# Optimization experiments

Measured on AMD Instinct MI355X. Metric: run time of the kernel, lower is better.

The kernel has to match this reference:

```python
import jax, jax.numpy as jnp
import numpy as np

NHEADS = 16
KVHEADS = 4
HEAD_DIM = 128  # emb_kq_per_head == emb_v_per_head
ROPE_THETA = 10000.0


def _rotary(x, cos, sin):
    # x: [B, S, H, D]; half-split rotation
    x1, x2 = jnp.split(x, 2, axis=-1)
    rot = jnp.concatenate([-x2, x1], axis=-1)
    return x * cos + rot * sin


def setup_inputs() -> dict:
    key = jax.random.key(0)
    k1, k2, k3 = jax.random.split(key, 3)
    B, S, E = 2, 2048, 2048
    qkv_out = NHEADS * HEAD_DIM + 2 * KVHEADS * HEAD_DIM  # 3072
    return {
        "x": jax.random.normal(k1, (B, S, E), dtype=jnp.float32),
        "w_qkv": jax.random.normal(k2, (E, qkv_out), dtype=jnp.float32) * 0.02,
        "w_dense": jax.random.normal(k3, (NHEADS * HEAD_DIM, E), dtype=jnp.float32) * 0.02,
    }


def reference(x, w_qkv, w_dense):
    B, S, E = x.shape
    D = HEAD_DIM
    # fused QKV projection (use_bias=False), then split per FusedQKV.splits
    qkv = x @ w_qkv  # [B, S, 3072]
    q, k, v = jnp.split(qkv, [NHEADS * D, NHEADS * D + KVHEADS * D], axis=-1)
    q = q.reshape(B, S, NHEADS, D)
    k = k.reshape(B, S, KVHEADS, D)
    v = v.reshape(B, S, KVHEADS, D)

    # rotary position encoding, positions = arange(S)
    pos = jnp.arange(S, dtype=jnp.float32)
    inv_freq = 1.0 / (ROPE_THETA ** (jnp.arange(0, D, 2, dtype=jnp.float32) / D))
    ang = pos[:, None] * inv_freq[None, :]                 # [S, D/2]
    ang = jnp.concatenate([ang, ang], axis=-1)             # [S, D]
    cos = jnp.cos(ang)[None, :, None, :]                   # [1, S, 1, D]
    sin = jnp.sin(ang)[None, :, None, :]
    q = _rotary(q, cos, sin)
    k = _rotary(k, cos, sin)

    # GQA: expand kv heads to query heads
    rep = NHEADS // KVHEADS
    k = jnp.repeat(k, rep, axis=2)  # [B, S, NHEADS, D]
    v = jnp.repeat(v, rep, axis=2)

    scale = 1.0 / jnp.sqrt(jnp.asarray(D, dtype=x.dtype))
    scores = jnp.einsum("bqhd,bkhd->bhqk", q, k) * scale   # [B, H, S, S]
    causal = jnp.tril(jnp.ones((S, S), dtype=bool))
    scores = jnp.where(causal[None, None], scores, jnp.finfo(scores.dtype).min)
    probs = jax.nn.softmax(scores, axis=-1)
    attn = jnp.einsum("bhqk,bkhd->bqhd", probs, v)         # [B, S, H, D]
    attn = attn.reshape(B, S, NHEADS * D)
    return attn @ w_dense                                  # [B, S, E]
```

## Files before the change

### kernel.cpp

```cpp
#include <hip/hip_runtime.h>
#include <type_traits>


typedef __attribute__((ext_vector_type(8))) short short8;
typedef __attribute__((ext_vector_type(4))) float floatx4;
typedef __attribute__((ext_vector_type(4))) unsigned short ushort4v;
typedef __attribute__((ext_vector_type(4))) unsigned int uint4v;

constexpr int NH    = 16;
constexpr int NKV   = 4;
constexpr int HD    = 128;
constexpr int SEQ   = 2048;
constexpr int EMB   = 2048;
constexpr int NBATCH = 2;
constexpr int MROWS = NBATCH * SEQ;
constexpr int NQKV  = (NH + 2 * NKV) * HD;

__device__ __forceinline__ unsigned short f2b(float f) {
  union { float f; unsigned u; } v; v.f = f;
  unsigned u = v.u + 0x7FFFu + ((v.u >> 16) & 1u);
  return (unsigned short)(u >> 16);
}
__device__ __forceinline__ float b2f(unsigned short h) {
  union { unsigned u; float f; } v; v.u = (unsigned)h << 16;
  return v.f;
}

__device__ __forceinline__ void gload_lds16(const unsigned short* g,
                                            unsigned short* lds) {
  __builtin_amdgcn_global_load_lds(
      (const __attribute__((address_space(1))) unsigned int*)g,
      (__attribute__((address_space(3))) unsigned int*)lds, 16, 0, 0);
}

constexpr int PREP_CVT   = 8192;
constexpr int PREP_TQKV  = PREP_CVT + 6144;
constexpr int PREP_TD    = PREP_TQKV + 4096;
constexpr int PREP_TOTAL = PREP_TD + 512;

__global__ __launch_bounds__(256) void prep(
    const float* __restrict__ x, unsigned short* __restrict__ xb,
    const float* __restrict__ wqkv, unsigned short* __restrict__ oqkv,
    const float* __restrict__ wd, unsigned short* __restrict__ od,
    float* __restrict__ rtab) {
  const int blk = blockIdx.x;
  const int tid = threadIdx.x;
  __shared__ float t[32][33];
  if (blk < PREP_CVT) {
    const int i = (blk * 256 + tid) * 4;
    floatx4 v = *(const floatx4*)(x + i);
    ushort4v o = { f2b(v[0]), f2b(v[1]), f2b(v[2]), f2b(v[3]) };
    *(ushort4v*)(xb + i) = o;
  } else if (blk < PREP_TD) {
    const float* in;
    unsigned short* out;
    int C, cx, ry;
    if (blk < PREP_TQKV) {
      const int local = blk - PREP_CVT;
      in = wqkv; out = oqkv; C = NQKV; cx = local % 96; ry = local / 96;
    } else {
      const int local = blk - PREP_TQKV;
      in = wd; out = od; C = EMB; cx = local % 64; ry = local / 64;
    }
    const int c0 = cx * 32, r0 = ry * 32;
    const int tx = tid & 31, ty = tid >> 5;
#pragma unroll
    for (int i = 0; i < 32; i += 8)
      t[ty + i][tx] = in[(long)(r0 + ty + i) * C + (c0 + tx)];
    __syncthreads();
#pragma unroll
    for (int i = 0; i < 32; i += 8)
      out[(long)(c0 + ty + i) * EMB + (r0 + tx)] = f2b(t[tx][ty + i]);
  } else {
    const int idx = (blk - PREP_TD) * 256 + tid;
    const int j = idx & 63, s = idx >> 6;
    const float e = -(float)j * (2.0f * 13.287712379549449f / 128.0f);
    const float ang = (float)s * exp2f(e);
    float sn, c;
    sincosf(ang, &sn, &c);
    rtab[idx * 2]     = c;
    rtab[idx * 2 + 1] = sn;
  }
}

constexpr int BM = 128, BK = 64;

template <int MODE>
__global__ __launch_bounds__(256, MODE == 1 ? 4 : 3) void gemm_bt(
    const unsigned short* __restrict__ A,
    const unsigned short* __restrict__ BT,
    int Mdim, int Ndim, int Kdim,
    float* __restrict__ outF,
    unsigned short* __restrict__ Qb,
    unsigned short* __restrict__ Kb,
    unsigned short* __restrict__ Vt,
    const float* __restrict__ ropetab,
    float qscale) {
  constexpr int TBN = (MODE == 1) ? 64 : 128;
  constexpr int NI  = TBN / 32;
  __shared__ __align__(16) unsigned short smem[BM * BK + TBN * BK];
  unsigned short (*As)[BK] = (unsigned short (*)[BK])smem;
  unsigned short (*Bs)[BK] = (unsigned short (*)[BK])(smem + BM * BK);
  const int tid = threadIdx.x;
  const int nwg = gridDim.x * gridDim.y;
  const int orig = blockIdx.x + gridDim.x * blockIdx.y;
  const int id = (orig & 7) * (nwg >> 3) + (orig >> 3);
  const int bm = (id / gridDim.x) * BM;
  const int bn = (id % gridDim.x) * TBN;
  const int wave = tid >> 6, lane = tid & 63;
  const int l = lane & 15, q = lane >> 4;
  const int l7 = l & 7;
  const int wm = (wave >> 1) * 64, wn = (wave & 1) * (TBN / 2);

  floatx4 acc[4][NI] = {};

  const int srow = lane >> 3;
  const int scol = ((lane & 7) ^ srow) * 8;
  const unsigned short* Arow = A + (long)bm * Kdim;
  const unsigned short* Brow = BT + (long)bn * Kdim;

  for (int k0 = 0; k0 < Kdim; k0 += BK) {
#pragma unroll
    for (int i = 0; i < 4; ++i) {
      const int r0 = wave * 32 + i * 8;
      gload_lds16(Arow + (long)(r0 + srow) * Kdim + k0 + scol, &As[r0][0]);
    }
#pragma unroll
    for (int i = 0; i < TBN / 32; ++i) {
      const int r0 = wave * (TBN / 4) + i * 8;
      gload_lds16(Brow + (long)(r0 + srow) * Kdim + k0 + scol, &Bs[r0][0]);
    }
    __syncthreads();
#pragma unroll
    for (int kk = 0; kk < 2; ++kk) {
      short8 af[4], bfr[NI];
#pragma unroll
      for (int mi = 0; mi < 4; ++mi)
        af[mi] = *(const short8*)&As[wm + mi * 16 + l][((kk * 4 + q) ^ l7) * 8];
#pragma unroll
      for (int ni = 0; ni < NI; ++ni)
        bfr[ni] = *(const short8*)&Bs[wn + ni * 16 + l][((kk * 4 + q) ^ l7) * 8];
#pragma unroll
      for (int mi = 0; mi < 4; ++mi)
#pragma unroll
        for (int ni = 0; ni < NI; ++ni)
          acc[mi][ni] = __builtin_amdgcn_mfma_f32_16x16x32_bf16(
              af[mi], bfr[ni], acc[mi][ni], 0, 0, 0);
    }
    __syncthreads();
  }

  if constexpr (MODE == 1) {
#pragma unroll
    for (int mi = 0; mi < 4; ++mi) {
      const int rowbase = bm + wm + mi * 16 + q * 4;
#pragma unroll
      for (int ni = 0; ni < NI; ++ni) {
        const int col = bn + wn + ni * 16 + l;
#pragma unroll
        for (int r = 0; r < 4; ++r)
          outF[(long)(rowbase + r) * Ndim + col] = acc[mi][ni][r];
      }
    }
    return;
  }

  unsigned short (*Ct)[128] = (unsigned short (*)[128])smem;
#pragma unroll
  for (int mi = 0; mi < 4; ++mi)
#pragma unroll
    for (int ni = 0; ni < NI; ++ni)
#pragma unroll
      for (int r = 0; r < 4; ++r) {
        const int row = wm + mi * 16 + q * 4 + r;
        const int col = wn + ni * 16 + l;
        const int cs = ((((col >> 3) ^ row) & 7) | (col & 64 ? 8 : 0)) * 8 + (col & 7);
        Ct[row][cs] = f2b(acc[mi][ni][r]);
      }
  __syncthreads();

  if (bn >= (NH + NKV) * HD) {
    const int hh = (bn - (NH + NKV) * HD) >> 7;
    const int d = tid >> 1, ch = tid & 1;
    const int m0 = bm + ch * 64;
    const int bb = m0 >> 11, sbase = m0 & (SEQ - 1);
    unsigned short* vrow =
        Vt + ((long)(bb * NKV + hh)) * HD * SEQ + (long)d * SEQ + sbase;
    const int dblk = d >> 3, dlo = d & 7, dhi = (d & 64) ? 8 : 0;
#pragma unroll
    for (int pb = 0; pb < 8; ++pb) {
      short8 ov;
#pragma unroll
      for (int j = 0; j < 8; ++j) {
        const int p6 = pb * 8 + j;
        const int s6 = (p6 & 32) | ((p6 & 24) >> 1) | ((p6 & 4) << 2) | (p6 & 3);
        const int row = ch * 64 + s6;
        const int cs = (((dblk ^ row) & 7) | dhi) * 8 + dlo;
        ov[j] = (short)Ct[row][cs];
      }
      *(short8*)(vrow + pb * 8) = ov;
    }
  } else {
    const int row = tid >> 1, g = tid & 1;
    const int m = bm + row, bb = m >> 11, s = m & (SEQ - 1);
    const bool isQ = (bn < NH * HD);
    unsigned short* dst;
    if (isQ) dst = Qb + (((long)(bb * NH + (bn >> 7))) * SEQ + s) * HD;
    else     dst = Kb + (((long)(bb * NKV + ((bn - NH * HD) >> 7))) * SEQ + s) * HD;
    const float scale = isQ ? qscale : 1.0f;
    const float* trow = ropetab + (long)s * 128;
#pragma unroll
    for (int i = 0; i < 8; ++i) {
      const int lbo = g * 8 + i;
      const int lbx = (g ^ 1) * 8 + i;
      const int pbo = (lbo & 8) | ((lbo ^ row) & 7);
      const int pbx = (lbx & 8) | ((lbx ^ row) & 7);
      short8 xo = *(const short8*)&Ct[row][pbo * 8];
      short8 xx = *(const short8*)&Ct[row][pbx * 8];
      floatx4 t0 = *(const floatx4*)(trow + i * 16);
      floatx4 t1 = *(const floatx4*)(trow + i * 16 + 4);
      floatx4 t2 = *(const floatx4*)(trow + i * 16 + 8);
      floatx4 t3 = *(const floatx4*)(trow + i * 16 + 12);
      const float cc[8] = { t0[0], t0[2], t1[0], t1[2], t2[0], t2[2], t3[0], t3[2] };
      const float ss[8] = { t0[1], t0[3], t1[1], t1[3], t2[1], t2[3], t3[1], t3[3] };
      short8 outv;
#pragma unroll
      for (int j2 = 0; j2 < 8; ++j2) {
        const float xown = b2f((unsigned short)xo[j2]);
        const float xoth = b2f((unsigned short)xx[j2]);
        const float rr = g ? (xown * cc[j2] + xoth * ss[j2])
                           : (xown * cc[j2] - xoth * ss[j2]);
        outv[j2] = (short)f2b(rr * scale);
      }
      *(short8*)(dst + g * 64 + i * 8) = outv;
    }
  }
}

__global__ __launch_bounds__(256, 2) void attn_kernel(
    const unsigned short* __restrict__ Q,
    const unsigned short* __restrict__ K,
    const unsigned short* __restrict__ VT,
    unsigned short* __restrict__ attn) {
  const int h = blockIdx.y, b = blockIdx.z;
  const int t = b ? (15 - (int)blockIdx.x) : (int)blockIdx.x;
  const int kvh = h >> 2;
  const int tid = threadIdx.x;
  const int wave = tid >> 6, lane = tid & 63;
  const int l = lane & 15, q = lane >> 4;
  const int l7 = l & 7;
  const int wq = wave * 32;

  const unsigned short* Kh  = K  + ((long)(b * NKV + kvh)) * SEQ * HD;
  const unsigned short* VTh = VT + ((long)(b * NKV + kvh)) * HD * SEQ;

  __shared__ __align__(16) unsigned short smem[2 * 64 * 128 + 2 * 128 * 64];
  unsigned short (*Ks)[64 * 128]  = (unsigned short (*)[64 * 128])smem;
  unsigned short (*VTs)[128 * 64] = (unsigned short (*)[128 * 64])(smem + 2 * 64 * 128);

  int koff[4], voff[4];
  {
    const int k_rl = lane >> 4, k_bp = lane & 15;
    const int v_rl = lane >> 3, v_bp = lane & 7;
#pragma unroll
    for (int j = 0; j < 4; ++j) {
      const int rk = (wave * 4 + j) * 4 + k_rl;
      koff[j] = rk * HD + (k_bp ^ (rk & 15)) * 8;
      const int rv = (wave * 4 + j) * 8 + v_rl;
      voff[j] = rv * SEQ + (v_bp ^ (rv & 7)) * 8;
    }
  }

  short8 onesf;
#pragma unroll
  for (int i = 0; i < 8; ++i) onesf[i] = (short)0x3F80;

  auto stage = [&](int c, int buf) {
    const unsigned short* kc = Kh + c * (64 * HD);
    const unsigned short* vc = VTh + c * 64;
#pragma unroll
    for (int j = 0; j < 4; ++j)
      gload_lds16(kc + koff[j], &Ks[buf][(wave * 4 + j) * 4 * 128]);
#pragma unroll
    for (int j = 0; j < 4; ++j)
      gload_lds16(vc + voff[j], &VTs[buf][(wave * 4 + j) * 8 * 64]);
  };

  const unsigned short* Qh = Q + (((long)(b * NH + h)) * SEQ + t * 128) * HD;
  short8 qf[2][4];
#pragma unroll
  for (int mh = 0; mh < 2; ++mh)
#pragma unroll
    for (int kk = 0; kk < 4; ++kk)
      qf[mh][kk] = *(const short8*)(Qh + (long)(wq + mh * 16 + l) * HD + kk * 32 + q * 8);

  floatx4 o[2][9] = {};

  auto chunk_body = [&](auto masked, int cur, int kv0) {
    constexpr bool MASKED = decltype(masked)::value;
    floatx4 sf[2][4] = {};
#pragma unroll
    for (int kk = 0; kk < 4; ++kk) {
      short8 kf[4];
#pragma unroll
      for (int ni = 0; ni < 4; ++ni)
        kf[ni] = *(const short8*)&Ks[cur][(ni * 16 + l) * 128 + (((kk * 4 + q) ^ l) * 8)];
      __builtin_amdgcn_s_setprio(1);
#pragma unroll
      for (int mh = 0; mh < 2; ++mh)
#pragma unroll
        for (int ni = 0; ni < 4; ++ni)
          sf[mh][ni] = __builtin_amdgcn_mfma_f32_16x16x32_bf16(
              kf[ni], qf[mh][kk], sf[mh][ni], 0, 0, 0);
      __builtin_amdgcn_s_setprio(0);
    }
    short8 pf[2][2];
#pragma unroll
    for (int mh = 0; mh < 2; ++mh) {
      const int qrow = t * 128 + wq + mh * 16 + l;
      unsigned u[8];
#pragma unroll
      for (int ni = 0; ni < 4; ++ni) {
        if constexpr (MASKED) {
#pragma unroll
          for (int r = 0; r < 4; ++r)
            if (kv0 + ni * 16 + q * 4 + r > qrow) sf[mh][ni][r] = -3e38f;
        }
        float e0 = exp2f(sf[mh][ni][0]);
        float e1 = exp2f(sf[mh][ni][1]);
        float e2 = exp2f(sf[mh][ni][2]);
        float e3 = exp2f(sf[mh][ni][3]);
        asm("v_cvt_pk_bf16_f32 %0, %1, %2" : "=v"(u[ni * 2]) : "v"(e0), "v"(e1));
        asm("v_cvt_pk_bf16_f32 %0, %1, %2" : "=v"(u[ni * 2 + 1]) : "v"(e2), "v"(e3));
      }
      union { uint4v v; short8 s; } a0, a1;
      a0.v = (uint4v){u[0], u[1], u[2], u[3]};
      a1.v = (uint4v){u[4], u[5], u[6], u[7]};
      pf[mh][0] = a0.s;
      pf[mh][1] = a1.s;
    }
#pragma unroll
    for (int c2 = 0; c2 < 2; ++c2) {
      const int pb = ((c2 * 4 + q) ^ l7) * 8;
      __builtin_amdgcn_s_setprio(1);
#pragma unroll
      for (int di = 0; di < 8; ++di) {
        short8 vf = *(const short8*)&VTs[cur][(di * 16 + l) * 64 + pb];
        o[0][di] = __builtin_amdgcn_mfma_f32_16x16x32_bf16(pf[0][c2], vf, o[0][di], 0, 0, 0);
        o[1][di] = __builtin_amdgcn_mfma_f32_16x16x32_bf16(pf[1][c2], vf, o[1][di], 0, 0, 0);
      }
      o[0][8] = __builtin_amdgcn_mfma_f32_16x16x32_bf16(pf[0][c2], onesf, o[0][8], 0, 0, 0);
      o[1][8] = __builtin_amdgcn_mfma_f32_16x16x32_bf16(pf[1][c2], onesf, o[1][8], 0, 0, 0);
      __builtin_amdgcn_s_setprio(0);
    }
  };

  const int nc = 2 * t + 2;
  stage(0, 0);
  __syncthreads();

  int c = 0;
#pragma unroll 1
  for (; c < nc - 2; ++c) {
    stage(c + 1, (c & 1) ^ 1);
    chunk_body(std::false_type{}, c & 1, c * 64);
    __syncthreads();
  }
  stage(c + 1, (c & 1) ^ 1);
  chunk_body(std::true_type{}, c & 1, c * 64);
  __syncthreads();
  ++c;
  chunk_body(std::true_type{}, c & 1, c * 64);
  __syncthreads();

  unsigned short (*Ob)[136] = (unsigned short (*)[136])smem;
#pragma unroll
  for (int mh = 0; mh < 2; ++mh)
#pragma unroll
    for (int r = 0; r < 4; ++r) {
      const float inv = 1.0f / o[mh][8][r];
#pragma unroll
      for (int di = 0; di < 8; ++di)
        Ob[wq + mh * 16 + q * 4 + r][di * 16 + l] = f2b(o[mh][di][r] * inv);
    }
  __syncthreads();
  {
    const int row = tid >> 1, g = (tid & 1) * 64;
    const int s = t * 128 + row;
    unsigned short* dst = attn + ((long)(b * SEQ + s)) * (NH * HD) + h * HD + g;
#pragma unroll
    for (int j = 0; j < 8; ++j)
      *(short8*)(dst + j * 8) = *(const short8*)&Ob[row][g + j * 8];
  }
}

extern "C" void kernel_launch(void* const* d_in, const int* in_sizes, int n_in,
                              void* d_out, int out_size, void* d_ws, size_t ws_size,
                              hipStream_t stream) {
  const float* x       = (const float*)d_in[0];
  const float* w_qkv   = (const float*)d_in[1];
  const float* w_dense = (const float*)d_in[2];
  float* out = (float*)d_out;

  char* ws = (char*)d_ws;
  const size_t MB = 1024 * 1024;
  unsigned short* xb    = (unsigned short*)(ws);
  unsigned short* wqkvT = (unsigned short*)(ws + 16 * MB);
  unsigned short* wdT   = (unsigned short*)(ws + 28 * MB);
  unsigned short* Qb    = (unsigned short*)(ws + 36 * MB);
  unsigned short* Kb    = (unsigned short*)(ws + 52 * MB);
  unsigned short* VTb   = (unsigned short*)(ws + 56 * MB);
  float*          rtab  = (float*)(ws + 60 * MB);
  unsigned short* attn  = xb;

  const float qscale = 0.08838834764831845f * 1.4426950408889634f;

  prep<<<PREP_TOTAL, 256, 0, stream>>>(x, xb, w_qkv, wqkvT, w_dense, wdT, rtab);

  gemm_bt<0><<<dim3(NQKV / 128, MROWS / BM), 256, 0, stream>>>(
      xb, wqkvT, MROWS, NQKV, EMB, nullptr, Qb, Kb, VTb, rtab, qscale);

  attn_kernel<<<dim3(16, NH, NBATCH), 256, 0, stream>>>(Qb, Kb, VTb, attn);

  gemm_bt<1><<<dim3(EMB / 64, MROWS / BM), 256, 0, stream>>>(
      attn, wdT, MROWS, EMB, NH * HD, out, nullptr, nullptr, nullptr, nullptr, 0.0f);
}
```

Before: 285.7 us.

## Fuse fp32-to-bf16 conversion of x into QKV GEMM operand load

Drops the separate pass in the prep kernel that converts x to bf16. The QKV GEMM now reads fp32 x directly into registers, packs it to bf16 with v_cvt_pk_bf16_f32 and stores it into the same swizzled LDS layout. The aim is to remove a full read and write of the activation tensor. The trade-off is that the A-tile loads become synchronous register loads instead of async global-to-LDS loads, and each tile moves twice the bytes. The change also removes the workgroup ID remap in the GEMM and the s_setprio hints around the MFMA blocks in the attention kernel.

```diff
diff --git a/kernel.cpp b/kernel.cpp
--- a/kernel.cpp
+++ b/kernel.cpp
@@ -33,31 +33,23 @@
       (__attribute__((address_space(3))) unsigned int*)lds, 16, 0, 0);
 }
 
-constexpr int PREP_CVT   = 8192;
-constexpr int PREP_TQKV  = PREP_CVT + 6144;
+constexpr int PREP_TQKV  = 6144;
 constexpr int PREP_TD    = PREP_TQKV + 4096;
 constexpr int PREP_TOTAL = PREP_TD + 512;
 
 __global__ __launch_bounds__(256) void prep(
-    const float* __restrict__ x, unsigned short* __restrict__ xb,
     const float* __restrict__ wqkv, unsigned short* __restrict__ oqkv,
     const float* __restrict__ wd, unsigned short* __restrict__ od,
     float* __restrict__ rtab) {
   const int blk = blockIdx.x;
   const int tid = threadIdx.x;
   __shared__ float t[32][33];
-  if (blk < PREP_CVT) {
-    const int i = (blk * 256 + tid) * 4;
-    floatx4 v = *(const floatx4*)(x + i);
-    ushort4v o = { f2b(v[0]), f2b(v[1]), f2b(v[2]), f2b(v[3]) };
-    *(ushort4v*)(xb + i) = o;
-  } else if (blk < PREP_TD) {
+  if (blk < PREP_TD) {
     const float* in;
     unsigned short* out;
     int C, cx, ry;
     if (blk < PREP_TQKV) {
-      const int local = blk - PREP_CVT;
-      in = wqkv; out = oqkv; C = NQKV; cx = local % 96; ry = local / 96;
+      in = wqkv; out = oqkv; C = NQKV; cx = blk % 96; ry = blk / 96;
     } else {
       const int local = blk - PREP_TQKV;
       in = wd; out = od; C = EMB; cx = local % 64; ry = local / 64;
@@ -87,6 +79,7 @@
 
 template <int MODE>
 __global__ __launch_bounds__(256, MODE == 1 ? 4 : 3) void gemm_bt(
+    const float* __restrict__ AF,
     const unsigned short* __restrict__ A,
     const unsigned short* __restrict__ BT,
     int Mdim, int Ndim, int Kdim,
@@ -102,11 +95,8 @@
   unsigned short (*As)[BK] = (unsigned short (*)[BK])smem;
   unsigned short (*Bs)[BK] = (unsigned short (*)[BK])(smem + BM * BK);
   const int tid = threadIdx.x;
-  const int nwg = gridDim.x * gridDim.y;
-  const int orig = blockIdx.x + gridDim.x * blockIdx.y;
-  const int id = (orig & 7) * (nwg >> 3) + (orig >> 3);
-  const int bm = (id / gridDim.x) * BM;
-  const int bn = (id % gridDim.x) * TBN;
+  const int bm = blockIdx.y * BM;
+  const int bn = blockIdx.x * TBN;
   const int wave = tid >> 6, lane = tid & 63;
   const int l = lane & 15, q = lane >> 4;
   const int l7 = l & 7;
@@ -116,14 +106,32 @@
 
   const int srow = lane >> 3;
   const int scol = ((lane & 7) ^ srow) * 8;
-  const unsigned short* Arow = A + (long)bm * Kdim;
   const unsigned short* Brow = BT + (long)bn * Kdim;
+  const float*          ArowF = AF + (long)bm * Kdim;
+  const unsigned short* ArowB = A + (long)bm * Kdim;
 
   for (int k0 = 0; k0 < Kdim; k0 += BK) {
-#pragma unroll
-    for (int i = 0; i < 4; ++i) {
-      const int r0 = wave * 32 + i * 8;
-      gload_lds16(Arow + (long)(r0 + srow) * Kdim + k0 + scol, &As[r0][0]);
+    if constexpr (MODE == 0) {
+#pragma unroll
+      for (int i = 0; i < 4; ++i) {
+        const int r0 = wave * 32 + i * 8;
+        const float* src = ArowF + (long)(r0 + srow) * Kdim + k0 + scol;
+        floatx4 a0 = *(const floatx4*)src;
+        floatx4 a1 = *(const floatx4*)(src + 4);
+        unsigned p0, p1, p2, p3;
+        asm("v_cvt_pk_bf16_f32 %0, %1, %2" : "=v"(p0) : "v"(a0[0]), "v"(a0[1]));
+        asm("v_cvt_pk_bf16_f32 %0, %1, %2" : "=v"(p1) : "v"(a0[2]), "v"(a0[3]));
+        asm("v_cvt_pk_bf16_f32 %0, %1, %2" : "=v"(p2) : "v"(a1[0]), "v"(a1[1]));
+        asm("v_cvt_pk_bf16_f32 %0, %1, %2" : "=v"(p3) : "v"(a1[2]), "v"(a1[3]));
+        uint4v w = { p0, p1, p2, p3 };
+        *(uint4v*)&As[r0 + srow][(lane & 7) * 8] = w;
+      }
+    } else {
+#pragma unroll
+      for (int i = 0; i < 4; ++i) {
+        const int r0 = wave * 32 + i * 8;
+        gload_lds16(ArowB + (long)(r0 + srow) * Kdim + k0 + scol, &As[r0][0]);
+      }
     }
 #pragma unroll
     for (int i = 0; i < TBN / 32; ++i) {
@@ -305,14 +313,12 @@
 #pragma unroll
       for (int ni = 0; ni < 4; ++ni)
         kf[ni] = *(const short8*)&Ks[cur][(ni * 16 + l) * 128 + (((kk * 4 + q) ^ l) * 8)];
-      __builtin_amdgcn_s_setprio(1);
 #pragma unroll
       for (int mh = 0; mh < 2; ++mh)
 #pragma unroll
         for (int ni = 0; ni < 4; ++ni)
           sf[mh][ni] = __builtin_amdgcn_mfma_f32_16x16x32_bf16(
               kf[ni], qf[mh][kk], sf[mh][ni], 0, 0, 0);
-      __builtin_amdgcn_s_setprio(0);
     }
     short8 pf[2][2];
 #pragma unroll
@@ -342,7 +348,6 @@
 #pragma unroll
     for (int c2 = 0; c2 < 2; ++c2) {
       const int pb = ((c2 * 4 + q) ^ l7) * 8;
-      __builtin_amdgcn_s_setprio(1);
 #pragma unroll
       for (int di = 0; di < 8; ++di) {
         short8 vf = *(const short8*)&VTs[cur][(di * 16 + l) * 64 + pb];
@@ -351,7 +356,6 @@
       }
       o[0][8] = __builtin_amdgcn_mfma_f32_16x16x32_bf16(pf[0][c2], onesf, o[0][8], 0, 0, 0);
       o[1][8] = __builtin_amdgcn_mfma_f32_16x16x32_bf16(pf[1][c2], onesf, o[1][8], 0, 0, 0);
-      __builtin_amdgcn_s_setprio(0);
     }
   };
 
@@ -404,24 +408,24 @@
 
   char* ws = (char*)d_ws;
   const size_t MB = 1024 * 1024;
-  unsigned short* xb    = (unsigned short*)(ws);
+  unsigned short* attnB = (unsigned short*)(ws);
   unsigned short* wqkvT = (unsigned short*)(ws + 16 * MB);
   unsigned short* wdT   = (unsigned short*)(ws + 28 * MB);
   unsigned short* Qb    = (unsigned short*)(ws + 36 * MB);
   unsigned short* Kb    = (unsigned short*)(ws + 52 * MB);
   unsigned short* VTb   = (unsigned short*)(ws + 56 * MB);
   float*          rtab  = (float*)(ws + 60 * MB);
-  unsigned short* attn  = xb;
 
   const float qscale = 0.08838834764831845f * 1.4426950408889634f;
 
-  prep<<<PREP_TOTAL, 256, 0, stream>>>(x, xb, w_qkv, wqkvT, w_dense, wdT, rtab);
+  prep<<<PREP_TOTAL, 256, 0, stream>>>(w_qkv, wqkvT, w_dense, wdT, rtab);
 
   gemm_bt<0><<<dim3(NQKV / 128, MROWS / BM), 256, 0, stream>>>(
-      xb, wqkvT, MROWS, NQKV, EMB, nullptr, Qb, Kb, VTb, rtab, qscale);
-
-  attn_kernel<<<dim3(16, NH, NBATCH), 256, 0, stream>>>(Qb, Kb, VTb, attn);
+      x, nullptr, wqkvT, MROWS, NQKV, EMB, nullptr, Qb, Kb, VTb, rtab, qscale);
+
+  attn_kernel<<<dim3(16, NH, NBATCH), 256, 0, stream>>>(Qb, Kb, VTb, attnB);
 
   gemm_bt<1><<<dim3(EMB / 64, MROWS / BM), 256, 0, stream>>>(
-      attn, wdT, MROWS, EMB, NH * HD, out, nullptr, nullptr, nullptr, nullptr, 0.0f);
-}
+      nullptr, attnB, wdT, MROWS, EMB, NH * HD, out, nullptr, nullptr, nullptr,
+      nullptr, 0.0f);
+}
```

After: 287.0 us. Within noise of the previous version (+0.5%).
